# Kernel tuning notes

Hardware: AMD Instinct MI355X
Metric: run time of the kernel (lower is better)

Reference implementation:

```python
import jax, jax.numpy as jnp
import numpy as np

B, N, D, F, H, C, L = 64, 8192, 5, 16, 4, 4, 4
NEG_SLOPE = 0.2


def setup_inputs() -> dict:
    key = jax.random.key(0)
    ks = jax.random.split(key, 16)
    lin = lambda k, fi, fo: (jax.random.normal(k, (fi, fo), jnp.float32) / np.sqrt(fi)).astype(jnp.float32)
    x = jax.random.normal(ks[0], (B, N, F), jnp.float32)
    agent_nodes = jax.random.randint(ks[1], (B,), 0, N, dtype=jnp.int32)
    neighbors = jax.random.randint(ks[2], (N, D), 0, N, dtype=jnp.int32)
    # GATv2 params (L layers, all 16 -> 4 heads x 4 = 16)
    Wl = jax.random.normal(ks[3], (L, F, H, C), jnp.float32) / np.sqrt(F)
    Wr = jax.random.normal(ks[4], (L, F, H, C), jnp.float32) / np.sqrt(F)
    att_w = jax.random.normal(ks[5], (L, H, C), jnp.float32) / np.sqrt(C)
    bias = jnp.zeros((L, H * C), jnp.float32)
    # global classifier 16->32->64, edge classifier 99->16->8->1
    Wg1, bg1 = lin(ks[6], H * C, 2 * H * C), jnp.zeros(2 * H * C, jnp.float32)
    Wg2, bg2 = lin(ks[7], 2 * H * C, 4 * H * C), jnp.zeros(4 * H * C, jnp.float32)
    e_in = 2 * H * C + 3 + 4 * H * C  # 99
    We1, be1 = lin(ks[8], e_in, H * C), jnp.zeros(H * C, jnp.float32)
    We2, be2 = lin(ks[9], H * C, H * C // 2), jnp.zeros(H * C // 2, jnp.float32)
    We3, be3 = lin(ks[10], H * C // 2, 1), jnp.zeros(1, jnp.float32)
    return dict(x=x, agent_nodes=agent_nodes, neighbors=neighbors, Wl=Wl, Wr=Wr,
                att_w=att_w, bias=bias, Wg1=Wg1, bg1=bg1, Wg2=Wg2, bg2=bg2,
                We1=We1, be1=be1, We2=We2, be2=be2, We3=We3, be3=be3)


def _gatv2_layer(h, src, dst, wl, wr, a, b, n_nodes):
    # h: [B,N,Fin]; wl/wr: [Fin,H,C]; a: [H,C]; b: [H*C]
    xl = jnp.einsum('bnf,fhc->bnhc', h, wl)   # source transform
    xr = jnp.einsum('bnf,fhc->bnhc', h, wr)   # target transform
    hs = xl[:, src]                            # [B,E,H,C]
    ht = xr[:, dst]
    logit = jnp.einsum('behc,hc->beh', jax.nn.leaky_relu(hs + ht, NEG_SLOPE), a)
    lt = logit.transpose(1, 0, 2)              # [E,B,H] (segment ops need E first)
    m = jax.ops.segment_max(lt, dst, num_segments=n_nodes)
    w = jnp.exp(lt - m[dst])
    s = jax.ops.segment_sum(w, dst, num_segments=n_nodes)
    alpha = w / (s[dst] + 1e-16)               # [E,B,H] softmax over in-edges of dst
    msg = alpha[..., None] * hs.transpose(1, 0, 2, 3)
    out = jax.ops.segment_sum(msg, dst, num_segments=n_nodes)  # [N,B,H,C]
    return out.transpose(1, 0, 2, 3).reshape(h.shape[0], n_nodes, -1) + b


def reference(x, agent_nodes, neighbors, Wl, Wr, att_w, bias,
              Wg1, bg1, Wg2, bg2, We1, be1, We2, be2, We3, be3):
    Bn, Nn, _ = x.shape
    Dd = neighbors.shape[1]
    loop = jnp.arange(Nn, dtype=neighbors.dtype)
    src = jnp.concatenate([jnp.repeat(loop, Dd), loop])   # add_self_loops
    dst = jnp.concatenate([neighbors.reshape(-1), loop])
    h = x
    for i in range(Wl.shape[0]):
        h = _gatv2_layer(h, src, dst, Wl[i], Wr[i], att_w[i], bias[i], Nn)
    # global mean aggregation -> 2 SlimFC(tanh)
    agg = jnp.tanh(h.mean(axis=1) @ Wg1 + bg1)
    agg = jnp.tanh(agg @ Wg2 + bg2)                        # [B,64]
    # agent out-edges: source node + its D neighbors
    nb = neighbors[agent_nodes]                            # [B,D]
    bi = jnp.arange(Bn)
    source = h[bi, agent_nodes]                            # [B,16]
    target = h[bi[:, None], nb]                            # [B,D,16]
    tok = jnp.eye(3, dtype=h.dtype)                        # 3 one-hot act tokens
    feats = jnp.concatenate([
        jnp.broadcast_to(source[:, None, None, :], (Bn, 3, Dd, source.shape[-1])),
        jnp.broadcast_to(tok[None, :, None, :], (Bn, 3, Dd, 3)),
        jnp.broadcast_to(target[:, None, :, :], (Bn, 3, Dd, target.shape[-1])),
        jnp.broadcast_to(agg[:, None, None, :], (Bn, 3, Dd, agg.shape[-1])),
    ], axis=-1)                                            # [B,3,D,99]
    e = jnp.tanh(feats @ We1 + be1)
    e = jnp.tanh(e @ We2 + be2)
    e = (e @ We3 + be3)[..., 0]                            # [B,3,D]
    # logits[b, turn*D + move] (convert_multidiscrete_action_to_discrete)
    return e.reshape(Bn, 3 * Dd)
```

## Files before the change

kernel.cpp:

```cpp
#include <hip/hip_runtime.h>
#include <hip/hip_fp16.h>
#include <cmath>

#define NNODES 8192
#define NB 64
#define ND 5
#define MAXDEG 64
#define NBLK_T0 2048
#define NBLK_LAY 2048



__global__ void __launch_bounds__(256)
k_t0fill(const float* __restrict__ x, const float* __restrict__ Wl0, const float* __restrict__ Wr0,
         __half* __restrict__ xl0, __half* __restrict__ xr0,
         const int* __restrict__ agent, const int* __restrict__ nbr,
         int* __restrict__ cnt, int* __restrict__ slot, int* __restrict__ needed) {
  if (blockIdx.x >= NBLK_T0) {
    int eb = blockIdx.x - NBLK_T0;
    if (eb < 160) {
      int i = eb*256 + threadIdx.x;
      int v = nbr[i];
      int pos = atomicAdd(&cnt[v], 1);
      slot[v*MAXDEG + 1 + pos] = i/ND;
    } else if (threadIdx.x < NB) {
      int an = agent[threadIdx.x];
      needed[an] = 1;
      #pragma unroll
      for (int d = 0; d < ND; ++d) needed[nbr[an*ND + d]] = 1;
    }
    return;
  }
  int gid = blockIdx.x*blockDim.x + threadIdx.x;
  int n = gid >> 6;
  int b = gid & 63;
  const float4* src = (const float4*)(x + (((size_t)b*NNODES + n) << 4));
  float hv[16];
  #pragma unroll
  for (int q = 0; q < 4; ++q) *(float4*)(hv+4*q) = src[q];
  float yl[16], yr[16];
  #pragma unroll
  for (int j = 0; j < 16; ++j) { yl[j] = 0.f; yr[j] = 0.f; }
  #pragma unroll
  for (int f = 0; f < 16; ++f) {
    float hf = hv[f];
    #pragma unroll
    for (int j = 0; j < 16; ++j) {
      yl[j] = fmaf(hf, Wl0[f*16+j], yl[j]);
      yr[j] = fmaf(hf, Wr0[f*16+j], yr[j]);
    }
  }
  size_t idx = ((size_t)n << 10) + (b << 4);
  __half2 lh[8], rh[8];
  #pragma unroll
  for (int j = 0; j < 8; ++j) {
    lh[j] = __floats2half2_rn(yl[2*j], yl[2*j+1]);
    rh[j] = __floats2half2_rn(yr[2*j], yr[2*j+1]);
  }
  float4* ld = (float4*)(xl0 + idx);
  ld[0] = *(float4*)&lh[0]; ld[1] = *(float4*)&lh[4];
  float4* rd = (float4*)(xr0 + idx);
  rd[0] = *(float4*)&rh[0]; rd[1] = *(float4*)&rh[4];
}


struct Row { float4 c0, c1; };

template<bool LAST>
__global__ void __launch_bounds__(256)
k_layer(const __half* __restrict__ xlin, const __half* __restrict__ xrin,
        __half* __restrict__ xlout, __half* __restrict__ xrout,
        const float* __restrict__ WlNext, const float* __restrict__ WrNext,
        const float* __restrict__ att, const float* __restrict__ bias,
        const int* __restrict__ cnt, const int* __restrict__ slot,
        const int* __restrict__ needed, __half* __restrict__ h,
        float* __restrict__ meanpart) {
  __shared__ float sW[544];
  int tid = threadIdx.x;
  int w = tid >> 6, lane = tid & 63;

  if (!LAST) {
    sW[tid]     = WlNext[tid];
    sW[256+tid] = WrNext[tid];
  }
  if (tid < 16)      sW[512+tid]    = att[tid];
  else if (tid < 32) sW[512+tid]    = bias[tid-16];
  __syncthreads();

  int v = (blockIdx.x << 2) + w;
  size_t loff = (size_t)(lane << 4);

  float aw[16];
  #pragma unroll
  for (int k = 0; k < 16; ++k) aw[k] = sW[512+k];

  float xrf[16];
  {
    const float4* p = (const float4*)(xrin + (((size_t)v) << 10) + loff);
    float4 c0 = p[0], c1 = p[1];
    __half2* ph0 = (__half2*)&c0;
    __half2* ph1 = (__half2*)&c1;
    #pragma unroll
    for (int j = 0; j < 4; ++j) {
      float2 f0 = __half22float2(ph0[j]);
      xrf[2*j]   = f0.x; xrf[2*j+1]   = f0.y;
      float2 f1 = __half22float2(ph1[j]);
      xrf[8+2*j] = f1.x; xrf[8+2*j+1] = f1.y;
    }
  }

  float s4[4] = {0.f, 0.f, 0.f, 0.f};
  float a[16];
  #pragma unroll
  for (int k = 0; k < 16; ++k) a[k] = 0.f;

  int deg = cnt[v];
  int tot = deg + 1;
  const int* sl = slot + v*MAXDEG;

  auto loadrow = [&](int u) -> Row {
    const float4* p = (const float4*)(xlin + (((size_t)u) << 10) + loff);
    Row r; r.c0 = p[0]; r.c1 = p[1]; return r;
  };
  auto process = [&](Row r) {
    float t[16];
    __half2* ph0 = (__half2*)&r.c0;
    __half2* ph1 = (__half2*)&r.c1;
    #pragma unroll
    for (int j = 0; j < 4; ++j) {
      float2 f0 = __half22float2(ph0[j]);
      t[2*j]   = f0.x; t[2*j+1]   = f0.y;
      float2 f1 = __half22float2(ph1[j]);
      t[8+2*j] = f1.x; t[8+2*j+1] = f1.y;
    }
    #pragma unroll
    for (int hd = 0; hd < 4; ++hd) {
      float z0 = t[4*hd+0] + xrf[4*hd+0]; z0 = (z0 >= 0.f) ? z0 : 0.2f*z0;
      float z1 = t[4*hd+1] + xrf[4*hd+1]; z1 = (z1 >= 0.f) ? z1 : 0.2f*z1;
      float z2 = t[4*hd+2] + xrf[4*hd+2]; z2 = (z2 >= 0.f) ? z2 : 0.2f*z2;
      float z3 = t[4*hd+3] + xrf[4*hd+3]; z3 = (z3 >= 0.f) ? z3 : 0.2f*z3;
      float lg = fmaf(z0, aw[4*hd+0], fmaf(z1, aw[4*hd+1],
                 fmaf(z2, aw[4*hd+2], z3*aw[4*hd+3])));
      float p = __expf(lg);
      s4[hd] += p;
      a[4*hd+0] = fmaf(p, t[4*hd+0], a[4*hd+0]);
      a[4*hd+1] = fmaf(p, t[4*hd+1], a[4*hd+1]);
      a[4*hd+2] = fmaf(p, t[4*hd+2], a[4*hd+2]);
      a[4*hd+3] = fmaf(p, t[4*hd+3], a[4*hd+3]);
    }
  };

  Row r0, r1, r2, r3, pA, pB;
  r0 = loadrow(v);
  if (tot > 1) r1 = loadrow(sl[1]);
  if (tot > 2) r2 = loadrow(sl[2]);
  if (tot > 3) r3 = loadrow(sl[3]);
  if (tot > 4) pA = loadrow(sl[4]);
  if (tot > 5) pB = loadrow(sl[5]);
  process(r0);
  if (tot > 1) process(r1);
  if (tot > 2) process(r2);
  if (tot > 3) process(r3);
  int e = 4;
  for (; e+1 < tot; e += 2) {
    Row cA = pA; if (e+2 < tot) pA = loadrow(sl[e+2]);
    Row cB = pB; if (e+3 < tot) pB = loadrow(sl[e+3]);
    process(cA); process(cB);
  }
  if (e < tot) process(pA);

  float o[16];
  #pragma unroll
  for (int hd = 0; hd < 4; ++hd) {
    float inv = 1.f / s4[hd];
    #pragma unroll
    for (int k = 0; k < 4; ++k)
      o[4*hd+k] = fmaf(a[4*hd+k], inv, sW[528+4*hd+k]);
  }

  if (!LAST) {
    float yl[16], yr[16];
    #pragma unroll
    for (int j = 0; j < 16; ++j) { yl[j] = 0.f; yr[j] = 0.f; }
    #pragma unroll
    for (int f = 0; f < 16; ++f) {
      float ofv = o[f];
      #pragma unroll
      for (int j4 = 0; j4 < 4; ++j4) {
        float4 wl4 = *(float4*)&sW[f*16 + j4*4];
        float4 wr4 = *(float4*)&sW[256 + f*16 + j4*4];
        yl[j4*4+0] = fmaf(ofv, wl4.x, yl[j4*4+0]);
        yl[j4*4+1] = fmaf(ofv, wl4.y, yl[j4*4+1]);
        yl[j4*4+2] = fmaf(ofv, wl4.z, yl[j4*4+2]);
        yl[j4*4+3] = fmaf(ofv, wl4.w, yl[j4*4+3]);
        yr[j4*4+0] = fmaf(ofv, wr4.x, yr[j4*4+0]);
        yr[j4*4+1] = fmaf(ofv, wr4.y, yr[j4*4+1]);
        yr[j4*4+2] = fmaf(ofv, wr4.z, yr[j4*4+2]);
        yr[j4*4+3] = fmaf(ofv, wr4.w, yr[j4*4+3]);
      }
    }
    __half2 lh[8], rh[8];
    #pragma unroll
    for (int j = 0; j < 8; ++j) {
      lh[j] = __floats2half2_rn(yl[2*j], yl[2*j+1]);
      rh[j] = __floats2half2_rn(yr[2*j], yr[2*j+1]);
    }
    size_t idx = (((size_t)v) << 10) + loff;
    float4* ld = (float4*)(xlout + idx);
    ld[0] = *(float4*)&lh[0]; ld[1] = *(float4*)&lh[4];
    float4* rd = (float4*)(xrout + idx);
    rd[0] = *(float4*)&rh[0]; rd[1] = *(float4*)&rh[4];
  } else {
    if (needed[v]) {
      __half2 hh[8];
      #pragma unroll
      for (int j = 0; j < 8; ++j) hh[j] = __floats2half2_rn(o[2*j], o[2*j+1]);
      float4* hd = (float4*)(h + (((size_t)v) << 10) + loff);
      hd[0] = *(float4*)&hh[0]; hd[1] = *(float4*)&hh[4];
    }
    __shared__ float msm[4][16][64];
    #pragma unroll
    for (int k = 0; k < 16; ++k) msm[w][k][lane] = o[k];
    __syncthreads();
    #pragma unroll
    for (int c = 0; c < 4; ++c) {
      int hc = c*4 + w;
      int b  = lane;
      float ssum = msm[0][hc][b] + msm[1][hc][b] + msm[2][hc][b] + msm[3][hc][b];
      meanpart[(size_t)blockIdx.x*1024 + hc*64 + b] = ssum;
    }
  }
}


__global__ void __launch_bounds__(256)
k_tail(const __half* __restrict__ h, const int* __restrict__ agent,
       const int* __restrict__ nbr, const float* __restrict__ meanpart,
       const float* __restrict__ Wg1, const float* __restrict__ bg1,
       const float* __restrict__ Wg2, const float* __restrict__ bg2,
       const float* __restrict__ We1, const float* __restrict__ be1,
       const float* __restrict__ We2, const float* __restrict__ be2,
       const float* __restrict__ We3, const float* __restrict__ be3,
       float* __restrict__ out) {
  int b = blockIdx.x;
  int t = threadIdx.x;
  __shared__ float red[256];
  __shared__ float mean[16], g1[32], aggs[64];
  __shared__ float srcv[16];
  __shared__ float tgt[5][16];
  __shared__ float e1s[15][16];
  __shared__ float e2s[15][8];
  int an = agent[b];

  {
    int hc = t & 15, grp = t >> 4;
    float s = 0.f;
    int base = grp*128;
    for (int p = 0; p < 128; ++p)
      s += meanpart[(size_t)(base+p)*1024 + hc*64 + b];
    red[t] = s;
    __syncthreads();
    if (t < 16) {
      float m = 0.f;
      for (int g = 0; g < 16; ++g) m += red[g*16 + t];
      mean[t] = m * (1.0f/NNODES);
    }
  }
  if (t >= 64 && t < 80) srcv[t-64] = __half2float(h[((size_t)an << 10) + (b << 4) + (t-64)]);
  if (t >= 96 && t < 176) {
    int d = (t-96)/16, k = (t-96)%16;
    int nn = nbr[an*ND + d];
    tgt[d][k] = __half2float(h[((size_t)nn << 10) + (b << 4) + k]);
  }
  __syncthreads();
  if (t < 32) {
    float a = bg1[t];
    for (int f = 0; f < 16; ++f) a = fmaf(mean[f], Wg1[f*32+t], a);
    g1[t] = tanhf(a);
  }
  __syncthreads();
  if (t < 64) {
    float a = bg2[t];
    for (int f = 0; f < 32; ++f) a = fmaf(g1[f], Wg2[f*64+t], a);
    aggs[t] = tanhf(a);
  }
  __syncthreads();
  if (t < 240) {
    int j = t & 15, td = t >> 4;
    int tk = td/5, d = td%5;
    float a = be1[j];
    for (int k = 0; k < 16; ++k) a = fmaf(srcv[k],  We1[k*16+j],      a);
    a += We1[(16+tk)*16 + j];
    for (int k = 0; k < 16; ++k) a = fmaf(tgt[d][k], We1[(19+k)*16+j], a);
    for (int k = 0; k < 64; ++k) a = fmaf(aggs[k],  We1[(35+k)*16+j], a);
    e1s[td][j] = tanhf(a);
  }
  __syncthreads();
  if (t < 120) {
    int j = t & 7, td = t >> 3;
    float a = be2[j];
    for (int k = 0; k < 16; ++k) a = fmaf(e1s[td][k], We2[k*8+j], a);
    e2s[td][j] = tanhf(a);
  }
  __syncthreads();
  if (t < 15) {
    float a = be3[0];
    for (int k = 0; k < 8; ++k) a = fmaf(e2s[t][k], We3[k], a);
    out[b*15 + t] = a;
  }
}


extern "C" void kernel_launch(void* const* d_in, const int* in_sizes, int n_in,
                              void* d_out, int out_size, void* d_ws, size_t ws_size,
                              hipStream_t stream) {
  const float* x     = (const float*)d_in[0];
  const int*   agent = (const int*)  d_in[1];
  const int*   nbr   = (const int*)  d_in[2];
  const float* Wl    = (const float*)d_in[3];
  const float* Wr    = (const float*)d_in[4];
  const float* att   = (const float*)d_in[5];
  const float* bias  = (const float*)d_in[6];
  const float* Wg1   = (const float*)d_in[7];
  const float* bg1   = (const float*)d_in[8];
  const float* Wg2   = (const float*)d_in[9];
  const float* bg2   = (const float*)d_in[10];
  const float* We1   = (const float*)d_in[11];
  const float* be1   = (const float*)d_in[12];
  const float* We2   = (const float*)d_in[13];
  const float* be2   = (const float*)d_in[14];
  const float* We3   = (const float*)d_in[15];
  const float* be3   = (const float*)d_in[16];
  float* out = (float*)d_out;

  char* ws = (char*)d_ws;
  size_t off = 0;
  auto alloc = [&](size_t bytes) -> void* {
    void* p = ws + off;
    off += (bytes + 255) & ~(size_t)255;
    return p;
  };
  const size_t XBYTES = (size_t)NNODES*NB*16*sizeof(__half);
  __half* h    = (__half*)alloc(XBYTES);
  __half* xlA  = (__half*)alloc(XBYTES);
  __half* xlB  = (__half*)alloc(XBYTES);
  __half* xrA  = (__half*)alloc(XBYTES);
  __half* xrB  = (__half*)alloc(XBYTES);
  int*  slot   = (int*)alloc((size_t)NNODES*MAXDEG*sizeof(int));
  float* meanpart = (float*)alloc((size_t)NBLK_LAY*1024*sizeof(float));
  int* cnt    = (int*)alloc(NNODES*sizeof(int));
  int* needed = (int*)alloc(NNODES*sizeof(int));

  hipMemsetAsync(cnt, 0, NNODES*sizeof(int)*2, stream);

  k_t0fill<<<NBLK_T0 + 161, 256, 0, stream>>>(x, Wl, Wr, xlA, xrA,
                                              agent, nbr, cnt, slot, needed);

  k_layer<false><<<NBLK_LAY, 256, 0, stream>>>(xlA, xrA, xlB, xrB, Wl + 256, Wr + 256,
                                               att,      bias,      cnt, slot, needed, nullptr, nullptr);
  k_layer<false><<<NBLK_LAY, 256, 0, stream>>>(xlB, xrB, xlA, xrA, Wl + 512, Wr + 512,
                                               att + 16, bias + 16, cnt, slot, needed, nullptr, nullptr);
  k_layer<false><<<NBLK_LAY, 256, 0, stream>>>(xlA, xrA, xlB, xrB, Wl + 768, Wr + 768,
                                               att + 32, bias + 32, cnt, slot, needed, nullptr, nullptr);
  k_layer<true ><<<NBLK_LAY, 256, 0, stream>>>(xlB, xrB, nullptr, nullptr, nullptr, nullptr,
                                               att + 48, bias + 48, cnt, slot, needed, h, meanpart);

  k_tail<<<NB, 256, 0, stream>>>(h, agent, nbr, meanpart,
                                 Wg1, bg1, Wg2, bg2,
                                 We1, be1, We2, be2, We3, be3, out);
}
```

Before: 274.5 us.

## Split each node's in-edges across four waves and reduce through shared memory

Each block now handles a single destination node, and its four waves each take a strided quarter of the in-edge list. Partial softmax numerators and denominators are combined in shared memory, and each wave then computes one head's output and the next-layer transform for that head. The last layer now writes the full h for every node, and the tail kernel computes the global mean from h directly, which removes the meanpart buffer and the needed mask. This shortens the serial gather chain per wave and exposes more parallelism. In exchange it adds block barriers, launches four times as many blocks, writes all of h in the final layer, and makes the tail do a larger reduction over only 64 blocks.

```diff
diff --git a/kernel.cpp b/kernel.cpp
--- a/kernel.cpp
+++ b/kernel.cpp
@@ -7,28 +7,23 @@
 #define ND 5
 #define MAXDEG 64
 #define NBLK_T0 2048
-#define NBLK_LAY 2048
-
+#define NBLK_LAY 8192
+
+
+struct RowV { float4 c0, c1; };
 
 
 __global__ void __launch_bounds__(256)
 k_t0fill(const float* __restrict__ x, const float* __restrict__ Wl0, const float* __restrict__ Wr0,
          __half* __restrict__ xl0, __half* __restrict__ xr0,
-         const int* __restrict__ agent, const int* __restrict__ nbr,
-         int* __restrict__ cnt, int* __restrict__ slot, int* __restrict__ needed) {
+         const int* __restrict__ nbr,
+         int* __restrict__ cnt, int* __restrict__ slot) {
   if (blockIdx.x >= NBLK_T0) {
     int eb = blockIdx.x - NBLK_T0;
-    if (eb < 160) {
-      int i = eb*256 + threadIdx.x;
-      int v = nbr[i];
-      int pos = atomicAdd(&cnt[v], 1);
-      slot[v*MAXDEG + 1 + pos] = i/ND;
-    } else if (threadIdx.x < NB) {
-      int an = agent[threadIdx.x];
-      needed[an] = 1;
-      #pragma unroll
-      for (int d = 0; d < ND; ++d) needed[nbr[an*ND + d]] = 1;
-    }
+    int i = eb*256 + threadIdx.x;
+    int v = nbr[i];
+    int pos = atomicAdd(&cnt[v], 1);
+    slot[v*MAXDEG + 1 + pos] = i/ND;
     return;
   }
   int gid = blockIdx.x*blockDim.x + threadIdx.x;
@@ -63,8 +58,6 @@
   rd[0] = *(float4*)&rh[0]; rd[1] = *(float4*)&rh[4];
 }
 
-
-struct Row { float4 c0, c1; };
 
 template<bool LAST>
 __global__ void __launch_bounds__(256)
@@ -73,9 +66,9 @@
         const float* __restrict__ WlNext, const float* __restrict__ WrNext,
         const float* __restrict__ att, const float* __restrict__ bias,
         const int* __restrict__ cnt, const int* __restrict__ slot,
-        const int* __restrict__ needed, __half* __restrict__ h,
-        float* __restrict__ meanpart) {
+        __half* __restrict__ h) {
   __shared__ float sW[544];
+  __shared__ float4 red4[5][4][64];
   int tid = threadIdx.x;
   int w = tid >> 6, lane = tid & 63;
 
@@ -83,11 +76,12 @@
     sW[tid]     = WlNext[tid];
     sW[256+tid] = WrNext[tid];
   }
-  if (tid < 16)      sW[512+tid]    = att[tid];
-  else if (tid < 32) sW[512+tid]    = bias[tid-16];
-  __syncthreads();
-
-  int v = (blockIdx.x << 2) + w;
+  if (tid < 16)      sW[512+tid] = att[tid];
+  else if (tid < 32) sW[512+tid] = bias[tid-16];
+  __syncthreads();
+
+  int v = blockIdx.x;
+  size_t base = ((size_t)v) << 10;
   size_t loff = (size_t)(lane << 4);
 
   float aw[16];
@@ -96,7 +90,7 @@
 
   float xrf[16];
   {
-    const float4* p = (const float4*)(xrin + (((size_t)v) << 10) + loff);
+    const float4* p = (const float4*)(xrin + base + loff);
     float4 c0 = p[0], c1 = p[1];
     __half2* ph0 = (__half2*)&c0;
     __half2* ph1 = (__half2*)&c1;
@@ -118,11 +112,17 @@
   int tot = deg + 1;
   const int* sl = slot + v*MAXDEG;
 
-  auto loadrow = [&](int u) -> Row {
+  int myn = (tot - w + 3) >> 2;
+
+  auto uat = [&](int i) -> int {
+    int r = w + 4*i;
+    return (r == 0) ? v : sl[r];
+  };
+  auto loadrow = [&](int u) -> RowV {
     const float4* p = (const float4*)(xlin + (((size_t)u) << 10) + loff);
-    Row r; r.c0 = p[0]; r.c1 = p[1]; return r;
+    RowV r; r.c0 = p[0]; r.c1 = p[1]; return r;
   };
-  auto process = [&](Row r) {
+  auto process = [&](RowV r) {
     float t[16];
     __half2* ph0 = (__half2*)&r.c0;
     __half2* ph1 = (__half2*)&r.c1;
@@ -150,92 +150,90 @@
     }
   };
 
-  Row r0, r1, r2, r3, pA, pB;
-  r0 = loadrow(v);
-  if (tot > 1) r1 = loadrow(sl[1]);
-  if (tot > 2) r2 = loadrow(sl[2]);
-  if (tot > 3) r3 = loadrow(sl[3]);
-  if (tot > 4) pA = loadrow(sl[4]);
-  if (tot > 5) pB = loadrow(sl[5]);
-  process(r0);
-  if (tot > 1) process(r1);
-  if (tot > 2) process(r2);
-  if (tot > 3) process(r3);
-  int e = 4;
-  for (; e+1 < tot; e += 2) {
-    Row cA = pA; if (e+2 < tot) pA = loadrow(sl[e+2]);
-    Row cB = pB; if (e+3 < tot) pB = loadrow(sl[e+3]);
+  RowV r0, r1, pA, pB;
+  if (myn > 0) r0 = loadrow(uat(0));
+  if (myn > 1) r1 = loadrow(uat(1));
+  if (myn > 2) pA = loadrow(uat(2));
+  if (myn > 3) pB = loadrow(uat(3));
+  if (myn > 0) process(r0);
+  if (myn > 1) process(r1);
+  int i = 2;
+  for (; i+1 < myn; i += 2) {
+    RowV cA = pA; if (i+2 < myn) pA = loadrow(uat(i+2));
+    RowV cB = pB; if (i+3 < myn) pB = loadrow(uat(i+3));
     process(cA); process(cB);
   }
-  if (e < tot) process(pA);
-
-  float o[16];
-  #pragma unroll
-  for (int hd = 0; hd < 4; ++hd) {
-    float inv = 1.f / s4[hd];
-    #pragma unroll
-    for (int k = 0; k < 4; ++k)
-      o[4*hd+k] = fmaf(a[4*hd+k], inv, sW[528+4*hd+k]);
-  }
-
-  if (!LAST) {
-    float yl[16], yr[16];
-    #pragma unroll
-    for (int j = 0; j < 16; ++j) { yl[j] = 0.f; yr[j] = 0.f; }
+  if (i < myn) process(pA);
+
+  red4[0][w][lane] = make_float4(a[0],  a[1],  a[2],  a[3]);
+  red4[1][w][lane] = make_float4(a[4],  a[5],  a[6],  a[7]);
+  red4[2][w][lane] = make_float4(a[8],  a[9],  a[10], a[11]);
+  red4[3][w][lane] = make_float4(a[12], a[13], a[14], a[15]);
+  red4[4][w][lane] = make_float4(s4[0], s4[1], s4[2], s4[3]);
+  __syncthreads();
+
+  int b = lane, q = w;
+  float4 t0 = red4[q][0][b], t1 = red4[q][1][b];
+  float4 t2 = red4[q][2][b], t3 = red4[q][3][b];
+  float aa0 = t0.x + t1.x + t2.x + t3.x;
+  float aa1 = t0.y + t1.y + t2.y + t3.y;
+  float aa2 = t0.z + t1.z + t2.z + t3.z;
+  float aa3 = t0.w + t1.w + t2.w + t3.w;
+  float ss = 0.f;
+  #pragma unroll
+  for (int ww = 0; ww < 4; ++ww) {
+    float4 sv = red4[4][ww][b];
+    float c = (q == 0) ? sv.x : (q == 1) ? sv.y : (q == 2) ? sv.z : sv.w;
+    ss += c;
+  }
+  float inv = 1.f / ss;
+  float4 bsv = *(float4*)&sW[528 + q*4];
+  float o0 = fmaf(aa0, inv, bsv.x), o1 = fmaf(aa1, inv, bsv.y);
+  float o2 = fmaf(aa2, inv, bsv.z), o3 = fmaf(aa3, inv, bsv.w);
+
+  if (LAST) {
+    float2 hv;
+    ((__half2*)&hv)[0] = __floats2half2_rn(o0, o1);
+    ((__half2*)&hv)[1] = __floats2half2_rn(o2, o3);
+    *(float2*)(h + base + (b << 4) + (q << 2)) = hv;
+  } else {
+    __syncthreads();
+    float4* po4 = &red4[0][0][0];
+    po4[q*64 + b] = make_float4(o0, o1, o2, o3);
+    __syncthreads();
+    float of[16];
+    #pragma unroll
+    for (int f4 = 0; f4 < 4; ++f4) {
+      float4 t = po4[f4*64 + b];
+      of[f4*4+0] = t.x; of[f4*4+1] = t.y; of[f4*4+2] = t.z; of[f4*4+3] = t.w;
+    }
+    float yl0=0.f, yl1=0.f, yl2=0.f, yl3=0.f;
+    float yr0=0.f, yr1=0.f, yr2=0.f, yr3=0.f;
     #pragma unroll
     for (int f = 0; f < 16; ++f) {
-      float ofv = o[f];
-      #pragma unroll
-      for (int j4 = 0; j4 < 4; ++j4) {
-        float4 wl4 = *(float4*)&sW[f*16 + j4*4];
-        float4 wr4 = *(float4*)&sW[256 + f*16 + j4*4];
-        yl[j4*4+0] = fmaf(ofv, wl4.x, yl[j4*4+0]);
-        yl[j4*4+1] = fmaf(ofv, wl4.y, yl[j4*4+1]);
-        yl[j4*4+2] = fmaf(ofv, wl4.z, yl[j4*4+2]);
-        yl[j4*4+3] = fmaf(ofv, wl4.w, yl[j4*4+3]);
-        yr[j4*4+0] = fmaf(ofv, wr4.x, yr[j4*4+0]);
-        yr[j4*4+1] = fmaf(ofv, wr4.y, yr[j4*4+1]);
-        yr[j4*4+2] = fmaf(ofv, wr4.z, yr[j4*4+2]);
-        yr[j4*4+3] = fmaf(ofv, wr4.w, yr[j4*4+3]);
-      }
-    }
-    __half2 lh[8], rh[8];
-    #pragma unroll
-    for (int j = 0; j < 8; ++j) {
-      lh[j] = __floats2half2_rn(yl[2*j], yl[2*j+1]);
-      rh[j] = __floats2half2_rn(yr[2*j], yr[2*j+1]);
-    }
-    size_t idx = (((size_t)v) << 10) + loff;
-    float4* ld = (float4*)(xlout + idx);
-    ld[0] = *(float4*)&lh[0]; ld[1] = *(float4*)&lh[4];
-    float4* rd = (float4*)(xrout + idx);
-    rd[0] = *(float4*)&rh[0]; rd[1] = *(float4*)&rh[4];
-  } else {
-    if (needed[v]) {
-      __half2 hh[8];
-      #pragma unroll
-      for (int j = 0; j < 8; ++j) hh[j] = __floats2half2_rn(o[2*j], o[2*j+1]);
-      float4* hd = (float4*)(h + (((size_t)v) << 10) + loff);
-      hd[0] = *(float4*)&hh[0]; hd[1] = *(float4*)&hh[4];
-    }
-    __shared__ float msm[4][16][64];
-    #pragma unroll
-    for (int k = 0; k < 16; ++k) msm[w][k][lane] = o[k];
-    __syncthreads();
-    #pragma unroll
-    for (int c = 0; c < 4; ++c) {
-      int hc = c*4 + w;
-      int b  = lane;
-      float ssum = msm[0][hc][b] + msm[1][hc][b] + msm[2][hc][b] + msm[3][hc][b];
-      meanpart[(size_t)blockIdx.x*1024 + hc*64 + b] = ssum;
-    }
+      float4 wl4 = *(float4*)&sW[f*16 + q*4];
+      float4 wr4 = *(float4*)&sW[256 + f*16 + q*4];
+      float ofv = of[f];
+      yl0 = fmaf(ofv, wl4.x, yl0); yl1 = fmaf(ofv, wl4.y, yl1);
+      yl2 = fmaf(ofv, wl4.z, yl2); yl3 = fmaf(ofv, wl4.w, yl3);
+      yr0 = fmaf(ofv, wr4.x, yr0); yr1 = fmaf(ofv, wr4.y, yr1);
+      yr2 = fmaf(ofv, wr4.z, yr2); yr3 = fmaf(ofv, wr4.w, yr3);
+    }
+    float2 lo, ro;
+    ((__half2*)&lo)[0] = __floats2half2_rn(yl0, yl1);
+    ((__half2*)&lo)[1] = __floats2half2_rn(yl2, yl3);
+    ((__half2*)&ro)[0] = __floats2half2_rn(yr0, yr1);
+    ((__half2*)&ro)[1] = __floats2half2_rn(yr2, yr3);
+    size_t idx = base + (b << 4) + (q << 2);
+    *(float2*)(xlout + idx) = lo;
+    *(float2*)(xrout + idx) = ro;
   }
 }
 
 
 __global__ void __launch_bounds__(256)
 k_tail(const __half* __restrict__ h, const int* __restrict__ agent,
-       const int* __restrict__ nbr, const float* __restrict__ meanpart,
+       const int* __restrict__ nbr,
        const float* __restrict__ Wg1, const float* __restrict__ bg1,
        const float* __restrict__ Wg2, const float* __restrict__ bg2,
        const float* __restrict__ We1, const float* __restrict__ be1,
@@ -244,7 +242,7 @@
        float* __restrict__ out) {
   int b = blockIdx.x;
   int t = threadIdx.x;
-  __shared__ float red[256];
+  __shared__ float4 sred[256];
   __shared__ float mean[16], g1[32], aggs[64];
   __shared__ float srcv[16];
   __shared__ float tgt[5][16];
@@ -252,25 +250,44 @@
   __shared__ float e2s[15][8];
   int an = agent[b];
 
-  {
-    int hc = t & 15, grp = t >> 4;
-    float s = 0.f;
-    int base = grp*128;
-    for (int p = 0; p < 128; ++p)
-      s += meanpart[(size_t)(base+p)*1024 + hc*64 + b];
-    red[t] = s;
-    __syncthreads();
-    if (t < 16) {
-      float m = 0.f;
-      for (int g = 0; g < 16; ++g) m += red[g*16 + t];
-      mean[t] = m * (1.0f/NNODES);
-    }
-  }
   if (t >= 64 && t < 80) srcv[t-64] = __half2float(h[((size_t)an << 10) + (b << 4) + (t-64)]);
   if (t >= 96 && t < 176) {
     int d = (t-96)/16, k = (t-96)%16;
     int nn = nbr[an*ND + d];
     tgt[d][k] = __half2float(h[((size_t)nn << 10) + (b << 4) + k]);
+  }
+
+  {
+    int vq = t >> 2, quad = t & 3;
+    const __half* hb = h + (b << 4) + (quad << 2);
+    float m0 = 0.f, m1 = 0.f, m2 = 0.f, m3 = 0.f;
+    #pragma unroll 8
+    for (int i = 0; i < 128; ++i) {
+      size_t vv = ((size_t)(vq + (i << 6))) << 10;
+      float2 pv = *(const float2*)(hb + vv);
+      __half2* ph = (__half2*)&pv;
+      float2 f0 = __half22float2(ph[0]), f1 = __half22float2(ph[1]);
+      m0 += f0.x; m1 += f0.y; m2 += f1.x; m3 += f1.y;
+    }
+    sred[t] = make_float4(m0, m1, m2, m3);
+  }
+  __syncthreads();
+  if (t < 64) {
+    float4 x0 = sred[t], x1 = sred[t+64], x2 = sred[t+128], x3 = sred[t+192];
+    sred[t] = make_float4(x0.x+x1.x+x2.x+x3.x, x0.y+x1.y+x2.y+x3.y,
+                          x0.z+x1.z+x2.z+x3.z, x0.w+x1.w+x2.w+x3.w);
+  }
+  __syncthreads();
+  if (t < 4) {
+    float4 acc = make_float4(0.f, 0.f, 0.f, 0.f);
+    for (int k = 0; k < 16; ++k) {
+      float4 xx = sred[k*4 + t];
+      acc.x += xx.x; acc.y += xx.y; acc.z += xx.z; acc.w += xx.w;
+    }
+    mean[t*4+0] = acc.x * (1.0f/NNODES);
+    mean[t*4+1] = acc.y * (1.0f/NNODES);
+    mean[t*4+2] = acc.z * (1.0f/NNODES);
+    mean[t*4+3] = acc.w * (1.0f/NNODES);
   }
   __syncthreads();
   if (t < 32) {
@@ -347,25 +364,23 @@
   __half* xrA  = (__half*)alloc(XBYTES);
   __half* xrB  = (__half*)alloc(XBYTES);
   int*  slot   = (int*)alloc((size_t)NNODES*MAXDEG*sizeof(int));
-  float* meanpart = (float*)alloc((size_t)NBLK_LAY*1024*sizeof(float));
-  int* cnt    = (int*)alloc(NNODES*sizeof(int));
-  int* needed = (int*)alloc(NNODES*sizeof(int));
-
-  hipMemsetAsync(cnt, 0, NNODES*sizeof(int)*2, stream);
-
-  k_t0fill<<<NBLK_T0 + 161, 256, 0, stream>>>(x, Wl, Wr, xlA, xrA,
-                                              agent, nbr, cnt, slot, needed);
+  int*  cnt    = (int*)alloc(NNODES*sizeof(int));
+
+  hipMemsetAsync(cnt, 0, NNODES*sizeof(int), stream);
+
+  k_t0fill<<<NBLK_T0 + 160, 256, 0, stream>>>(x, Wl, Wr, xlA, xrA,
+                                              nbr, cnt, slot);
 
   k_layer<false><<<NBLK_LAY, 256, 0, stream>>>(xlA, xrA, xlB, xrB, Wl + 256, Wr + 256,
-                                               att,      bias,      cnt, slot, needed, nullptr, nullptr);
+                                               att,      bias,      cnt, slot, nullptr);
   k_layer<false><<<NBLK_LAY, 256, 0, stream>>>(xlB, xrB, xlA, xrA, Wl + 512, Wr + 512,
-                                               att + 16, bias + 16, cnt, slot, needed, nullptr, nullptr);
+                                               att + 16, bias + 16, cnt, slot, nullptr);
   k_layer<false><<<NBLK_LAY, 256, 0, stream>>>(xlA, xrA, xlB, xrB, Wl + 768, Wr + 768,
-                                               att + 32, bias + 32, cnt, slot, needed, nullptr, nullptr);
+                                               att + 32, bias + 32, cnt, slot, nullptr);
   k_layer<true ><<<NBLK_LAY, 256, 0, stream>>>(xlB, xrB, nullptr, nullptr, nullptr, nullptr,
-                                               att + 48, bias + 48, cnt, slot, needed, h, meanpart);
-
-  k_tail<<<NB, 256, 0, stream>>>(h, agent, nbr, meanpart,
+                                               att + 48, bias + 48, cnt, slot, h);
+
+  k_tail<<<NB, 256, 0, stream>>>(h, agent, nbr,
                                  Wg1, bg1, Wg2, bg2,
                                  We1, be1, We2, be2, We3, be3, out);
 }
```

Measured after the change: 278.3 us. About the same (+1.4%).
